# Kernel optimization log

Hardware: AMD Instinct MI355X
Metric: run time of the kernel (lower is better)

## Reference

```python
import jax, jax.numpy as jnp
import numpy as np

B, T, N_IN, N = 64, 512, 256, 512

def setup_inputs() -> dict:
    key = jax.random.key(0)
    k1, k2, k3 = jax.random.split(key, 3)
    x = jax.random.normal(k1, (B, T, N_IN), dtype=jnp.float32)
    # match nn.Linear default init scale roughly (uniform +-1/sqrt(fan_in))
    W_ih = jax.random.uniform(k2, (N, N_IN), dtype=jnp.float32, minval=-1.0, maxval=1.0) / np.sqrt(N_IN)
    W_hh = jax.random.uniform(k3, (N, N), dtype=jnp.float32, minval=-1.0, maxval=1.0) / np.sqrt(N)
    return {"x": x, "W_ih": W_ih, "W_hh": W_hh}

def reference(x, W_ih, W_hh):
    # h_t = W_hh @ tanh(h_{t-1}) + W_ih @ x_t, h_0 = 0 (pre-activation hidden stored)
    # x: [B, T, n_in] (batch_first). Precompute input projections for all steps.
    xp = jnp.einsum('btc,nc->tbn', x, W_ih)  # [T, B, N]

    def step(h, xp_t):
        h_new = jnp.tanh(h) @ W_hh.T + xp_t  # [B, N]
        return h_new, h_new

    h0 = jnp.zeros((x.shape[0], W_hh.shape[0]), dtype=x.dtype)
    _, hs = jax.lax.scan(step, h0, xp)  # hs: [T, B, N]
    return jnp.swapaxes(hs, 0, 1)  # [B, T, N], batch_first output
```

## Files before the change

### kernel.cpp

```cpp
#include <hip/hip_runtime.h>
#include <hip/hip_bf16.h>
#include <stdint.h>

#define B_   64
#define T_   512
#define NIN_ 256
#define N_   512

typedef _Float16 half2_t __attribute__((ext_vector_type(2)));

#if defined(__has_builtin)
#if __has_builtin(__builtin_amdgcn_fdot2)
#define HAVE_FDOT2 1
#endif
#endif

__device__ __forceinline__ float dot2acc(unsigned int a, unsigned int b, float c) {
#ifdef HAVE_FDOT2
  return __builtin_amdgcn_fdot2(__builtin_bit_cast(half2_t, a),
                                __builtin_bit_cast(half2_t, b), c, false);
#else
  half2_t ha = __builtin_bit_cast(half2_t, a), hb = __builtin_bit_cast(half2_t, b);
  c += (float)ha[0] * (float)hb[0];
  c += (float)ha[1] * (float)hb[1];
  return c;
#endif
}

__device__ __forceinline__ float fast_tanh(float x) {
  float e = __expf(2.0f * x);
  return 1.0f - 2.0f / (e + 1.0f);
}

__global__ __launch_bounds__(256) void xproj(const float* __restrict__ x,
                                             const float* __restrict__ Wih,
                                             float* __restrict__ out) {
  const int tid = threadIdx.x;
  const int bm = blockIdx.x;
  const int bn = blockIdx.y;
  const int tm = tid & 15;
  const int tn = tid >> 4;
  const int m0 = bm << 7;
  const int n0 = bn << 7;

  __shared__ float xt[32][132];
  __shared__ float wt[32][132];

  float acc[8][8];
#pragma unroll
  for (int i = 0; i < 8; ++i)
#pragma unroll
    for (int j = 0; j < 8; ++j) acc[i][j] = 0.f;

  for (int ko = 0; ko < NIN_; ko += 32) {
#pragma unroll
    for (int it = 0; it < 4; ++it) {
      const int fidx = it * 256 + tid;
      const int mm = fidx >> 3;
      const int k4 = (fidx & 7) << 2;
      const float4 vx = *(const float4*)(x + (size_t)(m0 + mm) * NIN_ + ko + k4);
      xt[k4 + 0][mm] = vx.x; xt[k4 + 1][mm] = vx.y;
      xt[k4 + 2][mm] = vx.z; xt[k4 + 3][mm] = vx.w;
      const float4 vw = *(const float4*)(Wih + (size_t)(n0 + mm) * NIN_ + ko + k4);
      wt[k4 + 0][mm] = vw.x; wt[k4 + 1][mm] = vw.y;
      wt[k4 + 2][mm] = vw.z; wt[k4 + 3][mm] = vw.w;
    }
    __syncthreads();
#pragma unroll 4
    for (int kk = 0; kk < 32; ++kk) {
      float a[8], b[8];
      *(float4*)&a[0] = *(const float4*)&xt[kk][8 * tm];
      *(float4*)&a[4] = *(const float4*)&xt[kk][8 * tm + 4];
      *(float4*)&b[0] = *(const float4*)&wt[kk][8 * tn];
      *(float4*)&b[4] = *(const float4*)&wt[kk][8 * tn + 4];
#pragma unroll
      for (int i = 0; i < 8; ++i)
#pragma unroll
        for (int j = 0; j < 8; ++j) acc[i][j] = fmaf(a[i], b[j], acc[i][j]);
    }
    __syncthreads();
  }

#pragma unroll
  for (int i = 0; i < 8; ++i) {
    float4 v0 = make_float4(acc[i][0], acc[i][1], acc[i][2], acc[i][3]);
    float4 v1 = make_float4(acc[i][4], acc[i][5], acc[i][6], acc[i][7]);
    float* p = out + (size_t)(m0 + 8 * tm + i) * N_ + n0 + 8 * tn;
    *(float4*)p = v0;
    *((float4*)p + 1) = v1;
  }
}

__global__ __launch_bounds__(448, 2) void rnn_scan(const float* __restrict__ Whh,
                                                   float* __restrict__ out,
                                                   unsigned long long* __restrict__ ex) {
  const int blk = blockIdx.x;
  const int m = blk >> 6;
  const int b = blk & 63;
  const int tid = threadIdx.x;
  const int wv = tid >> 6;
  const int lane = tid & 63;

  __shared__ __align__(16) unsigned int thp[2][256];

  float* outb = out + (size_t)b * T_ * N_;
  unsigned long long* exb = ex + (size_t)b * 2 * 256;

  if (tid < 256) {
    float2 h0 = *(const float2*)(outb + 2 * tid);
    half2_t hp;
    hp[0] = (_Float16)fast_tanh(h0.x);
    hp[1] = (_Float16)fast_tanh(h0.y);
    thp[0][tid] = __builtin_bit_cast(unsigned int, hp);
  }

  if (wv < 4) {
    const int cl = tid;
    const int nn = cl >> 1;
    const int hh = cl & 1;
    const int gn = m * 128 + nn;
    const bool even = (hh == 0);
    const bool q0 = ((cl & 3) == 0);
    const int pidx = m * 64 + (cl >> 2);

    unsigned int w[128];
    {
      const float* wr = Whh + (size_t)gn * N_ + hh * 256;
#pragma unroll
      for (int j = 0; j < 128; ++j) {
        half2_t h;
        h[0] = (_Float16)wr[2 * j];
        h[1] = (_Float16)wr[2 * j + 1];
        w[j] = __builtin_bit_cast(unsigned int, h);
      }
    }
    __syncthreads();

    for (int t = 1; t < T_; ++t) {
      float xp = 0.f;
      if (even) xp = outb[(size_t)t * N_ + gn];

      const uint4* tq = (const uint4*)&thp[(t - 1) & 1][hh * 128];
      float acc = 0.f;
#pragma unroll
      for (int j4 = 0; j4 < 32; ++j4) {
        uint4 tv = tq[j4];
        acc = dot2acc(w[4 * j4 + 0], tv.x, acc);
        acc = dot2acc(w[4 * j4 + 1], tv.y, acc);
        acc = dot2acc(w[4 * j4 + 2], tv.z, acc);
        acc = dot2acc(w[4 * j4 + 3], tv.w, acc);
      }
      float y = acc + __shfl_xor(acc, 1) + xp;
      float th = 0.f;
      if (even) th = fast_tanh(y);
      float thn = __shfl_xor(th, 2);
      if (q0) {
        half2_t hp;
        hp[0] = (_Float16)th;
        hp[1] = (_Float16)thn;
        const unsigned int pk = __builtin_bit_cast(unsigned int, hp);
        thp[t & 1][pidx] = pk;
        __hip_atomic_store(&exb[(t & 1) * 256 + pidx],
                           ((unsigned long long)(unsigned int)t << 32) | pk,
                           __ATOMIC_RELAXED, __HIP_MEMORY_SCOPE_AGENT);
      }
      if (even) __builtin_nontemporal_store(y, &outb[(size_t)t * N_ + gn]);
      __syncthreads();
    }
  } else {
    const int s = (wv - 4) * 64 + lane;
    const int pr = s + (s >= m * 64 ? 64 : 0);
    __syncthreads();

    for (int t = 1; t < T_; ++t) {
      if (t < T_ - 1) {
        unsigned long long v;
        do {
          v = __hip_atomic_load(&exb[(t & 1) * 256 + pr], __ATOMIC_RELAXED,
                                __HIP_MEMORY_SCOPE_AGENT);
        } while ((unsigned int)(v >> 32) != (unsigned int)t);
        thp[t & 1][pr] = (unsigned int)v;
      }
      __syncthreads();
    }
  }
}

extern "C" void kernel_launch(void* const* d_in, const int* in_sizes, int n_in,
                              void* d_out, int out_size, void* d_ws, size_t ws_size,
                              hipStream_t stream) {
  const float* x   = (const float*)d_in[0];
  const float* Wih = (const float*)d_in[1];
  const float* Whh = (const float*)d_in[2];
  float* out = (float*)d_out;
  unsigned long long* ex = (unsigned long long*)d_ws;

  hipMemsetAsync(d_ws, 0, (size_t)B_ * 2 * 256 * 8, stream);

  dim3 g1(256, 4);
  xproj<<<g1, 256, 0, stream>>>(x, Wih, out);
  rnn_scan<<<256, 448, 0, stream>>>(Whh, out, ex);
}
```

Measured before the change: 892.1 us.

## Run one block per batch row, dropping cross-block exchange and streaming the W_hh tail

The recurrent scan moves from four cooperating blocks per batch row, which swapped tanh values through global atomics and spin-waits, to a single 512-thread block per batch row in which each thread owns one output neuron. Each thread keeps 192 packed fp16 weight pairs in registers and reads the remaining 64 pairs from a pre-packed global copy on every step. A small new kernel packs W_hh to fp16 up front, and the workspace memset is removed. This removes the inter-block polling latency but uses only 64 blocks, does twice the dot-product work per thread, and adds per-step global weight reads.

```diff
diff --git a/kernel.cpp b/kernel.cpp
--- a/kernel.cpp
+++ b/kernel.cpp
@@ -6,6 +6,8 @@
 #define T_   512
 #define NIN_ 256
 #define N_   512
+#define PP   192
+#define GP   64
 
 typedef _Float16 half2_t __attribute__((ext_vector_type(2)));
 
@@ -32,6 +34,20 @@
   return 1.0f - 2.0f / (e + 1.0f);
 }
 
+__device__ __forceinline__ unsigned int packh2(float a, float b) {
+  half2_t h;
+  h[0] = (_Float16)a;
+  h[1] = (_Float16)b;
+  return __builtin_bit_cast(unsigned int, h);
+}
+
+__global__ __launch_bounds__(256) void packw(const float* __restrict__ Whh,
+                                             unsigned int* __restrict__ pw) {
+  const int i = blockIdx.x * 256 + threadIdx.x;
+  float2 v = *(const float2*)(Whh + 2 * (size_t)i);
+  pw[i] = packh2(v.x, v.y);
+}
+
 __global__ __launch_bounds__(256) void xproj(const float* __restrict__ x,
                                              const float* __restrict__ Wih,
                                              float* __restrict__ out) {
@@ -91,98 +107,81 @@
   }
 }
 
-__global__ __launch_bounds__(448, 2) void rnn_scan(const float* __restrict__ Whh,
-                                                   float* __restrict__ out,
-                                                   unsigned long long* __restrict__ ex) {
-  const int blk = blockIdx.x;
-  const int m = blk >> 6;
-  const int b = blk & 63;
-  const int tid = threadIdx.x;
-  const int wv = tid >> 6;
-  const int lane = tid & 63;
-
-  __shared__ __align__(16) unsigned int thp[2][256];
-
+__global__ __launch_bounds__(512, 2) void rnn_scan(const unsigned int* __restrict__ pw,
+                                                   float* __restrict__ out) {
+  const int b = blockIdx.x;
+  const int n = threadIdx.x;
   float* outb = out + (size_t)b * T_ * N_;
-  unsigned long long* exb = ex + (size_t)b * 2 * 256;
-
-  if (tid < 256) {
-    float2 h0 = *(const float2*)(outb + 2 * tid);
-    half2_t hp;
-    hp[0] = (_Float16)fast_tanh(h0.x);
-    hp[1] = (_Float16)fast_tanh(h0.y);
-    thp[0][tid] = __builtin_bit_cast(unsigned int, hp);
-  }
-
-  if (wv < 4) {
-    const int cl = tid;
-    const int nn = cl >> 1;
-    const int hh = cl & 1;
-    const int gn = m * 128 + nn;
-    const bool even = (hh == 0);
-    const bool q0 = ((cl & 3) == 0);
-    const int pidx = m * 64 + (cl >> 2);
-
-    unsigned int w[128];
-    {
-      const float* wr = Whh + (size_t)gn * N_ + hh * 256;
-#pragma unroll
-      for (int j = 0; j < 128; ++j) {
-        half2_t h;
-        h[0] = (_Float16)wr[2 * j];
-        h[1] = (_Float16)wr[2 * j + 1];
-        w[j] = __builtin_bit_cast(unsigned int, h);
-      }
-    }
+
+  const uint4* pwr = (const uint4*)(pw + (size_t)n * (N_ / 2));
+  unsigned int w[PP];
+#pragma unroll
+  for (int j4 = 0; j4 < PP / 4; ++j4) {
+    uint4 v = pwr[j4];
+    w[4 * j4 + 0] = v.x; w[4 * j4 + 1] = v.y;
+    w[4 * j4 + 2] = v.z; w[4 * j4 + 3] = v.w;
+  }
+  const uint4* gwr = pwr + PP / 4;
+
+  __shared__ __align__(16) unsigned int thp[2][N_ / 2];
+
+  if (n < 256) {
+    float2 h0 = *(const float2*)(outb + 2 * n);
+    thp[0][n] = packh2(fast_tanh(h0.x), fast_tanh(h0.y));
+  }
+  __syncthreads();
+
+  for (int t = 1; t < T_; ++t) {
+    float xp = outb[(size_t)t * N_ + n];
+
+    const uint4* tq = (const uint4*)thp[(t - 1) & 1];
+    float acc = 0.f;
+
+#pragma unroll
+    for (int j4 = 0; j4 < PP / 4; ++j4) {
+      uint4 tv = tq[j4];
+      acc = dot2acc(w[4 * j4 + 0], tv.x, acc);
+      acc = dot2acc(w[4 * j4 + 1], tv.y, acc);
+      acc = dot2acc(w[4 * j4 + 2], tv.z, acc);
+      acc = dot2acc(w[4 * j4 + 3], tv.w, acc);
+    }
+
+#pragma unroll 1
+    for (int c = 0; c < 4; ++c) {
+      uint4 g0 = gwr[4 * c + 0];
+      uint4 g1 = gwr[4 * c + 1];
+      uint4 g2 = gwr[4 * c + 2];
+      uint4 g3 = gwr[4 * c + 3];
+      uint4 t0 = tq[PP / 4 + 4 * c + 0];
+      uint4 t1 = tq[PP / 4 + 4 * c + 1];
+      uint4 t2 = tq[PP / 4 + 4 * c + 2];
+      uint4 t3 = tq[PP / 4 + 4 * c + 3];
+      acc = dot2acc(g0.x, t0.x, acc);
+      acc = dot2acc(g0.y, t0.y, acc);
+      acc = dot2acc(g0.z, t0.z, acc);
+      acc = dot2acc(g0.w, t0.w, acc);
+      acc = dot2acc(g1.x, t1.x, acc);
+      acc = dot2acc(g1.y, t1.y, acc);
+      acc = dot2acc(g1.z, t1.z, acc);
+      acc = dot2acc(g1.w, t1.w, acc);
+      acc = dot2acc(g2.x, t2.x, acc);
+      acc = dot2acc(g2.y, t2.y, acc);
+      acc = dot2acc(g2.z, t2.z, acc);
+      acc = dot2acc(g2.w, t2.w, acc);
+      acc = dot2acc(g3.x, t3.x, acc);
+      acc = dot2acc(g3.y, t3.y, acc);
+      acc = dot2acc(g3.z, t3.z, acc);
+      acc = dot2acc(g3.w, t3.w, acc);
+    }
+
+    const float y = acc + xp;
+    const float th = fast_tanh(y);
+    __builtin_nontemporal_store(y, &outb[(size_t)t * N_ + n]);
+
+    const float thn = __shfl_xor(th, 1);
+    if ((n & 1) == 0) thp[t & 1][n >> 1] = packh2(th, thn);
+
     __syncthreads();
-
-    for (int t = 1; t < T_; ++t) {
-      float xp = 0.f;
-      if (even) xp = outb[(size_t)t * N_ + gn];
-
-      const uint4* tq = (const uint4*)&thp[(t - 1) & 1][hh * 128];
-      float acc = 0.f;
-#pragma unroll
-      for (int j4 = 0; j4 < 32; ++j4) {
-        uint4 tv = tq[j4];
-        acc = dot2acc(w[4 * j4 + 0], tv.x, acc);
-        acc = dot2acc(w[4 * j4 + 1], tv.y, acc);
-        acc = dot2acc(w[4 * j4 + 2], tv.z, acc);
-        acc = dot2acc(w[4 * j4 + 3], tv.w, acc);
-      }
-      float y = acc + __shfl_xor(acc, 1) + xp;
-      float th = 0.f;
-      if (even) th = fast_tanh(y);
-      float thn = __shfl_xor(th, 2);
-      if (q0) {
-        half2_t hp;
-        hp[0] = (_Float16)th;
-        hp[1] = (_Float16)thn;
-        const unsigned int pk = __builtin_bit_cast(unsigned int, hp);
-        thp[t & 1][pidx] = pk;
-        __hip_atomic_store(&exb[(t & 1) * 256 + pidx],
-                           ((unsigned long long)(unsigned int)t << 32) | pk,
-                           __ATOMIC_RELAXED, __HIP_MEMORY_SCOPE_AGENT);
-      }
-      if (even) __builtin_nontemporal_store(y, &outb[(size_t)t * N_ + gn]);
-      __syncthreads();
-    }
-  } else {
-    const int s = (wv - 4) * 64 + lane;
-    const int pr = s + (s >= m * 64 ? 64 : 0);
-    __syncthreads();
-
-    for (int t = 1; t < T_; ++t) {
-      if (t < T_ - 1) {
-        unsigned long long v;
-        do {
-          v = __hip_atomic_load(&exb[(t & 1) * 256 + pr], __ATOMIC_RELAXED,
-                                __HIP_MEMORY_SCOPE_AGENT);
-        } while ((unsigned int)(v >> 32) != (unsigned int)t);
-        thp[t & 1][pr] = (unsigned int)v;
-      }
-      __syncthreads();
-    }
   }
 }
 
@@ -193,11 +192,10 @@
   const float* Wih = (const float*)d_in[1];
   const float* Whh = (const float*)d_in[2];
   float* out = (float*)d_out;
-  unsigned long long* ex = (unsigned long long*)d_ws;
-
-  hipMemsetAsync(d_ws, 0, (size_t)B_ * 2 * 256 * 8, stream);
-
+  unsigned int* pw = (unsigned int*)d_ws;
+
+  packw<<<512, 256, 0, stream>>>(Whh, pw);
   dim3 g1(256, 4);
   xproj<<<g1, 256, 0, stream>>>(x, Wih, out);
-  rnn_scan<<<256, 448, 0, stream>>>(Whh, out, ex);
-}
+  rnn_scan<<<B_, 512, 0, stream>>>(pw, out);
+}
```

Result: slower. 2.451 ms (+174.8%).

## Unify compute and poll warps in RNN scan, remap blocks to XCDs

Applied to the files above, without the earlier changes.

Replaces the split producer/poller warp design with 512 threads that each compute a quarter-row dot product over 64 packed weights, then poll peer blocks' published pre-activations themselves. Each block now publishes raw fp32 pre-activations; consumers apply tanh and pack to half2 into a swizzled shared layout. Block-to-batch mapping is changed so the four blocks of a batch share an XCD (blk&7), keeping cross-block exchange within one L2. This cuts register pressure and the per-step serial chain, in exchange for more exchange traffic, a tanh at every consumer, and a 2-slot ring whose correctness relies on the per-step syncs.

```diff
diff --git a/kernel.cpp b/kernel.cpp
--- a/kernel.cpp
+++ b/kernel.cpp
@@ -32,6 +32,17 @@
   return 1.0f - 2.0f / (e + 1.0f);
 }
 
+__device__ __forceinline__ unsigned int packh2(float a, float b) {
+  half2_t h;
+  h[0] = (_Float16)a;
+  h[1] = (_Float16)b;
+  return __builtin_bit_cast(unsigned int, h);
+}
+
+__device__ __forceinline__ int thp_idx(int p) {
+  return (((p >> 2) & 15) << 4) + ((p >> 6) << 2) + (p & 3);
+}
+
 __global__ __launch_bounds__(256) void xproj(const float* __restrict__ x,
                                              const float* __restrict__ Wih,
                                              float* __restrict__ out) {
@@ -91,98 +102,90 @@
   }
 }
 
-__global__ __launch_bounds__(448, 2) void rnn_scan(const float* __restrict__ Whh,
-                                                   float* __restrict__ out,
-                                                   unsigned long long* __restrict__ ex) {
+__global__ __launch_bounds__(512) void rnn_scan(const float* __restrict__ Whh,
+                                                float* __restrict__ out,
+                                                unsigned long long* __restrict__ ex) {
   const int blk = blockIdx.x;
-  const int m = blk >> 6;
-  const int b = blk & 63;
+  const int xcd = blk & 7;
+  const int rest = blk >> 3;
+  const int m = rest & 3;
+  const int b = xcd + ((rest >> 2) << 3);
   const int tid = threadIdx.x;
   const int wv = tid >> 6;
   const int lane = tid & 63;
+  const int q = lane & 3;
+  const int nn = wv * 16 + (lane >> 2);
+  const int gn = m * 128 + nn;
 
   __shared__ __align__(16) unsigned int thp[2][256];
 
   float* outb = out + (size_t)b * T_ * N_;
-  unsigned long long* exb = ex + (size_t)b * 2 * 256;
+  unsigned long long* exb = ex + (size_t)b * 1024;
+
+  unsigned int w[64];
+  {
+    const float* wr = Whh + (size_t)gn * N_ + q * 128;
+#pragma unroll
+    for (int j = 0; j < 64; ++j) {
+      float2 v = *(const float2*)(wr + 2 * j);
+      w[j] = packh2(v.x, v.y);
+    }
+  }
 
   if (tid < 256) {
     float2 h0 = *(const float2*)(outb + 2 * tid);
-    half2_t hp;
-    hp[0] = (_Float16)fast_tanh(h0.x);
-    hp[1] = (_Float16)fast_tanh(h0.y);
-    thp[0][tid] = __builtin_bit_cast(unsigned int, hp);
-  }
-
-  if (wv < 4) {
-    const int cl = tid;
-    const int nn = cl >> 1;
-    const int hh = cl & 1;
-    const int gn = m * 128 + nn;
-    const bool even = (hh == 0);
-    const bool q0 = ((cl & 3) == 0);
-    const int pidx = m * 64 + (cl >> 2);
-
-    unsigned int w[128];
-    {
-      const float* wr = Whh + (size_t)gn * N_ + hh * 256;
-#pragma unroll
-      for (int j = 0; j < 128; ++j) {
-        half2_t h;
-        h[0] = (_Float16)wr[2 * j];
-        h[1] = (_Float16)wr[2 * j + 1];
-        w[j] = __builtin_bit_cast(unsigned int, h);
-      }
+    thp[0][thp_idx(tid)] = packh2(fast_tanh(h0.x), fast_tanh(h0.y));
+  }
+
+  const int pv = tid & 127;
+  const int sr = tid >> 7;
+  const int sm = sr + (sr >= m ? 1 : 0);
+  const int prn = sm * 128 + pv;
+
+  __syncthreads();
+
+  for (int t = 1; t < T_; ++t) {
+    float xp = 0.f;
+    if (q == 0) xp = outb[(size_t)t * N_ + gn];
+
+    if (t >= 2 && tid < 384) {
+      unsigned long long v;
+      do {
+        v = __hip_atomic_load(&exb[((t - 1) & 1) * 512 + prn],
+                              __ATOMIC_RELAXED, __HIP_MEMORY_SCOPE_AGENT);
+      } while ((unsigned int)(v >> 32) != (unsigned int)(t - 1));
+      const float th = fast_tanh(__uint_as_float((unsigned int)v));
+      const float thn = __shfl_xor(th, 1);
+      if ((tid & 1) == 0) thp[(t - 1) & 1][thp_idx(prn >> 1)] = packh2(th, thn);
     }
     __syncthreads();
 
-    for (int t = 1; t < T_; ++t) {
-      float xp = 0.f;
-      if (even) xp = outb[(size_t)t * N_ + gn];
-
-      const uint4* tq = (const uint4*)&thp[(t - 1) & 1][hh * 128];
-      float acc = 0.f;
-#pragma unroll
-      for (int j4 = 0; j4 < 32; ++j4) {
-        uint4 tv = tq[j4];
-        acc = dot2acc(w[4 * j4 + 0], tv.x, acc);
-        acc = dot2acc(w[4 * j4 + 1], tv.y, acc);
-        acc = dot2acc(w[4 * j4 + 2], tv.z, acc);
-        acc = dot2acc(w[4 * j4 + 3], tv.w, acc);
-      }
-      float y = acc + __shfl_xor(acc, 1) + xp;
-      float th = 0.f;
-      if (even) th = fast_tanh(y);
-      float thn = __shfl_xor(th, 2);
-      if (q0) {
-        half2_t hp;
-        hp[0] = (_Float16)th;
-        hp[1] = (_Float16)thn;
-        const unsigned int pk = __builtin_bit_cast(unsigned int, hp);
-        thp[t & 1][pidx] = pk;
-        __hip_atomic_store(&exb[(t & 1) * 256 + pidx],
-                           ((unsigned long long)(unsigned int)t << 32) | pk,
-                           __ATOMIC_RELAXED, __HIP_MEMORY_SCOPE_AGENT);
-      }
-      if (even) __builtin_nontemporal_store(y, &outb[(size_t)t * N_ + gn]);
-      __syncthreads();
-    }
-  } else {
-    const int s = (wv - 4) * 64 + lane;
-    const int pr = s + (s >= m * 64 ? 64 : 0);
-    __syncthreads();
-
-    for (int t = 1; t < T_; ++t) {
-      if (t < T_ - 1) {
-        unsigned long long v;
-        do {
-          v = __hip_atomic_load(&exb[(t & 1) * 256 + pr], __ATOMIC_RELAXED,
-                                __HIP_MEMORY_SCOPE_AGENT);
-        } while ((unsigned int)(v >> 32) != (unsigned int)t);
-        thp[t & 1][pr] = (unsigned int)v;
-      }
-      __syncthreads();
-    }
+    const uint4* tq = (const uint4*)&thp[(t - 1) & 1][0];
+    float acc = 0.f;
+#pragma unroll
+    for (int j4 = 0; j4 < 16; ++j4) {
+      const uint4 tv = tq[j4 * 4 + q];
+      acc = dot2acc(w[4 * j4 + 0], tv.x, acc);
+      acc = dot2acc(w[4 * j4 + 1], tv.y, acc);
+      acc = dot2acc(w[4 * j4 + 2], tv.z, acc);
+      acc = dot2acc(w[4 * j4 + 3], tv.w, acc);
+    }
+    acc += __shfl_xor(acc, 1);
+    acc += __shfl_xor(acc, 2);
+
+    float th_own = 0.f;
+    if (q == 0) {
+      const float y = acc + xp;
+      __hip_atomic_store(&exb[(t & 1) * 512 + gn],
+                         ((unsigned long long)(unsigned int)t << 32) |
+                             (unsigned long long)__float_as_uint(y),
+                         __ATOMIC_RELAXED, __HIP_MEMORY_SCOPE_AGENT);
+      __builtin_nontemporal_store(y, &outb[(size_t)t * N_ + gn]);
+      th_own = fast_tanh(y);
+    }
+    const float th_nb = __shfl_xor(th_own, 4);
+    if ((lane & 7) == 0)
+      thp[t & 1][thp_idx(gn >> 1)] = packh2(th_own, th_nb);
   }
 }
 
@@ -195,9 +198,9 @@
   float* out = (float*)d_out;
   unsigned long long* ex = (unsigned long long*)d_ws;
 
-  hipMemsetAsync(d_ws, 0, (size_t)B_ * 2 * 256 * 8, stream);
+  hipMemsetAsync(d_ws, 0, (size_t)B_ * 2 * 512 * 8, stream);
 
   dim3 g1(256, 4);
   xproj<<<g1, 256, 0, stream>>>(x, Wih, out);
-  rnn_scan<<<256, 448, 0, stream>>>(Whh, out, ex);
-}
+  rnn_scan<<<256, 512, 0, stream>>>(Whh, out, ex);
+}
```

After: 760.2 us. 14.8% less time.
